# Performance work log

Hardware: AMD Instinct MI355X
Metric: run time of the kernel (lower is better)

The kernel has to match this reference:

```python
import jax, jax.numpy as jnp
import numpy as np
import math
from jax import lax

NUM_POS = 128        # random_choice in pos_neg_sampling
NUM_TOT = 256        # pos + (128 + negative_padding) always totals 256
POS_W = 10.0         # positive_weight in compute_loss


def _conv(x, w, b, pad):
    y = lax.conv_general_dilated(x, w, (1, 1), pad,
                                 dimension_numbers=('NCHW', 'OIHW', 'NCHW'))
    return y + b[None, :, None, None]


def make_anchor_box(img_h, img_w, gh, gw):
    # torch.range(0, W, W/(gw-1)) == inclusive linspace with gw points
    xs = jnp.linspace(0.0, float(img_w), gw)
    ys = jnp.linspace(0.0, float(img_h), gh)
    gx, gy = jnp.meshgrid(xs, ys, indexing='ij')          # (gw, gh) like torch.meshgrid
    xy = jnp.stack([gx.reshape(-1), gy.reshape(-1)], -1).reshape(gh, gw, 2)
    whs = []
    for area in (128 * 128, 256 * 256, 512 * 512):
        for wr, hr in ((1, 1), (2, 1), (1, 2)):
            u = math.sqrt(area / (wr * hr))
            whs.append((wr * u, hr * u))
    wh = jnp.asarray(whs, jnp.float32)                    # (9, 2)
    xy9 = jnp.broadcast_to(xy[:, :, None, :], (gh, gw, 9, 2))
    wh9 = jnp.broadcast_to(wh[None, None], (gh, gw, 9, 2))
    boxes = jnp.concatenate([xy9, xy9 + wh9], -1)         # x1,y1,x2,y2
    return boxes.reshape(-1, 4)


def pairwise_iou(t, a):
    # t: [T,4], a: [A,4], xyxy -> [T,A]
    lt = jnp.maximum(t[:, None, :2], a[None, :, :2])
    rb = jnp.minimum(t[:, None, 2:], a[None, :, 2:])
    wh = jnp.clip(rb - lt, 0.0)
    inter = wh[..., 0] * wh[..., 1]
    at = (t[:, 2] - t[:, 0]) * (t[:, 3] - t[:, 1])
    aa = (a[:, 2] - a[:, 0]) * (a[:, 3] - a[:, 1])
    return inter / (at[:, None] + aa[None, :] - inter)


def box_encode(anchor, bbox):
    awh = anchor[:, 2:] - anchor[:, :2]
    bwh = bbox[:, 2:] - bbox[:, :2]
    ac = anchor[:, :2] + awh / 2
    bc = bbox[:, :2] + bwh / 2
    dxy = (bc - ac) / awh
    dwh = jnp.log(bwh / awh)
    return jnp.concatenate([dxy, dwh], 1)


def rpn_forward(x, target, conv_w, conv_b, bbox_w, bbox_b, score_w, score_b,
                img_h, img_w):
    gh, gw = x.shape[-2], x.shape[-1]
    h = jax.nn.relu(_conv(x[None], conv_w, conv_b, 'SAME'))
    bbox = jax.nn.relu(_conv(h, bbox_w, bbox_b, 'VALID')).reshape(-1, 4)   # [A,4]
    score = jax.nn.relu(_conv(h, score_w, score_b, 'VALID')).reshape(-1, 2)  # [A,2]
    anchors = make_anchor_box(img_h, img_w, gh, gw)                        # [A,4]

    iou = pairwise_iou(target, anchors)                                    # [T,A]
    max_iou = iou.max(0)
    tgt_idx = jnp.argmax(iou, 0)

    # deterministic replacement for np.random.choice sampling (fixed shapes)
    pos_score = jnp.where(max_iou > 0.7, max_iou, -1.0)
    pos_vals, pos_idx = lax.top_k(pos_score, NUM_POS)
    pos_valid = pos_vals > 0.0
    n_pos = jnp.sum(pos_valid.astype(jnp.int32))

    neg_score = jnp.where(max_iou < 0.3, 1.0 - max_iou, -1.0)
    neg_vals, neg_idx = lax.top_k(neg_score, NUM_TOT)
    neg_valid = (neg_vals > 0.0) & (jnp.arange(NUM_TOT) < (NUM_TOT - n_pos))

    bbox_pred = bbox[pos_idx]                                              # [128,4]
    scores_sel = score[jnp.concatenate([pos_idx, neg_idx])]                # [384,2]
    valid = jnp.concatenate([pos_valid, neg_valid]).astype(jnp.float32)

    tgt_scores = jnp.concatenate([
        jnp.tile(jnp.asarray([[1.0, 0.0]], jnp.float32), (NUM_POS, 1)),
        jnp.tile(jnp.asarray([[0.0, 1.0]], jnp.float32), (NUM_TOT, 1))], 0)

    matched = target[tgt_idx[pos_idx]]
    treg = box_encode(anchors[pos_idx], matched)

    ce = -jnp.sum(tgt_scores * jax.nn.log_softmax(scores_sel, -1), -1)
    score_loss = jnp.sum(ce * valid) / jnp.maximum(jnp.sum(valid), 1.0)

    d = bbox_pred - treg
    sl1 = jnp.where(jnp.abs(d) < 1.0, 0.5 * d * d, jnp.abs(d) - 0.5)
    pm = pos_valid.astype(jnp.float32)[:, None]
    reg_loss = jnp.sum(sl1 * pm) / jnp.maximum(jnp.sum(pm) * 4.0, 1.0)

    return score_loss + POS_W * reg_loss


def setup_inputs():
    key = jax.random.key(0)
    ks = jax.random.split(key, 8)
    cin, gh, gw, nt = 512, 128, 128, 64
    x = jax.random.normal(ks[0], (cin, gh, gw), jnp.float32)
    cxy = jax.random.uniform(ks[1], (nt, 2), minval=300.0, maxval=1748.0)
    wh = jax.random.uniform(ks[2], (nt, 2), minval=64.0, maxval=512.0)
    target = jnp.concatenate([cxy - wh / 2, cxy + wh / 2], -1)
    conv_w = jax.random.normal(ks[3], (cin, cin, 3, 3), jnp.float32) * 0.02
    conv_b = jnp.zeros((cin,), jnp.float32)
    bbox_w = jax.random.normal(ks[4], (36, cin, 1, 1), jnp.float32) * 0.02
    bbox_b = jnp.zeros((36,), jnp.float32)
    score_w = jax.random.normal(ks[5], (18, cin, 1, 1), jnp.float32) * 0.02
    score_b = jnp.zeros((18,), jnp.float32)
    return {'x': x, 'target': target, 'conv_w': conv_w, 'conv_b': conv_b,
            'bbox_w': bbox_w, 'bbox_b': bbox_b, 'score_w': score_w,
            'score_b': score_b, 'img_h': 2048, 'img_w': 2048}


def reference(x, target, conv_w, conv_b, bbox_w, bbox_b, score_w, score_b,
              img_h, img_w):
    return rpn_forward(x, target, conv_w, conv_b, bbox_w, bbox_b,
                       score_w, score_b, img_h, img_w)
```

## Files before the change

kernel.cpp:

```cpp
#include <hip/hip_runtime.h>
#include <cstdint>
#include <cstddef>

typedef unsigned long long ull;
typedef __bf16 bf16x8 __attribute__((ext_vector_type(8)));
typedef float f32x4 __attribute__((ext_vector_type(4)));

#define NA     147456
#define NT     64
#define KDIM   4608
#define NTASK  1280
#define CAND_CAP 4096
#define KSPLIT 2
#define NSTEP  72
#define NIOUB  576
#define NTRB   2048
#define NPREP2 512
#define NZERO  197

#define OFF_WB2   0
#define OFF_XT    4718592
#define OFF_ZERO  22024192
#define OFF_H4    22302720
#define OFF_MIOU  32788480
#define OFF_CAND  33378304
#define OFF_CPB   34557952
#define OFF_CBZ   34560256
#define OFF_NPOS  34562560
#define OFF_TREG  34562576
#define OFF_TASKS 34564624

#define UANC 90.509667991878f
__device__ __constant__ float WKa[9] = {128.0f, 2.0f*UANC, UANC, 256.0f, 4.0f*UANC, 2.0f*UANC, 512.0f, 8.0f*UANC, 4.0f*UANC};
__device__ __constant__ float HKa[9] = {128.0f, UANC, 2.0f*UANC, 256.0f, 2.0f*UANC, 4.0f*UANC, 512.0f, 4.0f*UANC, 8.0f*UANC};

__device__ __forceinline__ float iou_one(float x1, float y1, float x2, float y2, float4 t) {
#pragma clang fp contract(off)
  float ltx = fmaxf(t.x, x1), lty = fmaxf(t.y, y1);
  float rbx = fminf(t.z, x2), rby = fminf(t.w, y2);
  float wx = fmaxf(rbx - ltx, 0.0f);
  float wy = fmaxf(rby - lty, 0.0f);
  float inter = wx * wy;
  float at = (t.z - t.x) * (t.w - t.y);
  float aa = (x2 - x1) * (y2 - y1);
  return inter / ((at + aa) - inter);
}

__device__ __forceinline__ unsigned short f2bf(float f) {
  unsigned int u = __float_as_uint(f);
  unsigned int r = (u + 0x7fffu + ((u >> 16) & 1u)) >> 16;
  return (unsigned short)r;
}

__device__ __forceinline__ int boff(int kcb) {
  int rk = kcb >> 6;
  int dy = (rk * 11) >> 5;
  int dxo = rk - dy * 3;
  return (dy * 130 + dxo) * 512 + (kcb & 63) * 8;
}

__global__ __launch_bounds__(256) void k_pi(const float* __restrict__ cw,
    unsigned short* __restrict__ Wb2, const float* __restrict__ x,
    unsigned short* __restrict__ xtb, unsigned short* __restrict__ zrg,
    const float* __restrict__ tgt, const int* __restrict__ imw,
    const int* __restrict__ imh, float* __restrict__ miou,
    ull* __restrict__ cand, int* __restrict__ cpb, int* __restrict__ cbz,
    float* __restrict__ out0) {
  __shared__ __align__(16) char smem[20480];
  int blk = blockIdx.x;
  int tid = threadIdx.x;
  if (blk >= NIOUB + NTRB + NPREP2) {
    int g = (blk - (NIOUB + NTRB + NPREP2)) * 256 + tid;
    uint4 z = {0u, 0u, 0u, 0u};
    if (g == 0) *out0 = 0.0f;
    if (g < 17408) {
      *(uint4*)(zrg + g * 8) = z;
    } else {
      int h = g - 17408;
      int pixi = h >> 6, j = h & 63;
      int yy, xx;
      if (pixi < 260) { yy = (pixi < 130) ? 0 : 129; xx = (pixi < 130) ? pixi : pixi - 130; }
      else { int p2 = pixi - 260; if (p2 < 128) { yy = 1 + p2; xx = 0; } else { yy = p2 - 127; xx = 129; } }
      *(uint4*)(xtb + (size_t)(yy * 130 + xx) * 512 + j * 8) = z;
    }
    return;
  }
  if (blk >= NIOUB + NTRB) {
    float* row = (float*)smem;
    int m = blk - (NIOUB + NTRB);
    const float* src = cw + (size_t)m * KDIM;
    for (int f = tid; f < KDIM; f += 256) {
      int cin = f / 9;
      row[cin * 10 + (f - cin * 9)] = src[f];
    }
    __syncthreads();
    for (int kc = tid; kc < 576; kc += 256) {
      int r = kc >> 6, c8 = kc & 63;
      int base = c8 * 80 + r;
      unsigned short o[8];
      #pragma unroll
      for (int j = 0; j < 8; ++j) o[j] = f2bf(row[base + j * 10]);
      *(uint4*)(Wb2 + ((size_t)kc * 512 + m) * 8) = *(const uint4*)o;
    }
    return;
  }
  if (blk >= NIOUB) {
    float* tile = (float*)smem;
    int tb = blk - NIOUB;
    int pix0 = (tb & 255) * 64;
    int cin0 = (tb >> 8) * 64;
    int pr = tid & 15, cr = tid >> 4;
    #pragma unroll
    for (int i = 0; i < 4; ++i) {
      int cin = cr + i * 16;
      float4 v = *(const float4*)(x + (size_t)(cin0 + cin) * 16384 + pix0 + pr * 4);
      tile[cin * 65 + pr * 4 + 0] = v.x;
      tile[cin * 65 + pr * 4 + 1] = v.y;
      tile[cin * 65 + pr * 4 + 2] = v.z;
      tile[cin * 65 + pr * 4 + 3] = v.w;
    }
    __syncthreads();
    #pragma unroll
    for (int i = 0; i < 4; ++i) {
      int pix = cr + i * 16;
      int plin = pix0 + pix;
      int py = plin >> 7, px = plin & 127;
      unsigned short o[4] = {f2bf(tile[(pr * 4 + 0) * 65 + pix]),
                             f2bf(tile[(pr * 4 + 1) * 65 + pix]),
                             f2bf(tile[(pr * 4 + 2) * 65 + pix]),
                             f2bf(tile[(pr * 4 + 3) * 65 + pix])};
      *(uint2*)(xtb + (size_t)((py + 1) * 130 + (px + 1)) * 512 + cin0 + pr * 4) = *(const uint2*)o;
    }
    return;
  }
  float4* ts = (float4*)smem;
  int* wz = (int*)(smem + 1024);
  int* wc = wz + 4;
  if (tid < NT) ts[tid] = ((const float4*)tgt)[tid];
  __syncthreads();
  int a = blk * 256 + tid;
  int k = a % 9;
  int pq = a / 9;
  int p = pq >> 7, q = pq & 127;
  float dx = (float)(*imw) / 127.0f;
  float dyl = (float)(*imh) / 127.0f;
  float x1 = (float)p * dx, y1 = (float)q * dyl;
  float x2 = x1 + WKa[k], y2 = y1 + HKa[k];
  float best = -1.0f;
  #pragma unroll 8
  for (int t = 0; t < NT; ++t) best = fmaxf(best, iou_one(x1, y1, x2, y2, ts[t]));
  miou[a] = best;
  int lane = tid & 63, w = tid >> 6;
  ull bz = __ballot(best == 0.0f);
  bool isc = best > 0.7f;
  ull bc = __ballot(isc);
  if (lane == 0) { wz[w] = (int)__popcll(bz); wc[w] = (int)__popcll(bc); }
  __syncthreads();
  if (tid == 0) {
    cbz[blk] = wz[0] + wz[1] + wz[2] + wz[3];
    cpb[blk] = wc[0] + wc[1] + wc[2] + wc[3];
  }
  if (isc) {
    int woff = 0;
    for (int i = 0; i < w; ++i) woff += wc[i];
    int rank = woff + (int)__popcll(bc & ((1ull << lane) - 1ull));
    cand[blk * 256 + rank] = ((ull)__float_as_uint(best) << 32) | (ull)(0xFFFFFFFFu - (unsigned)a);
  }
}

__global__ __launch_bounds__(256) void k_mfma(const unsigned short* __restrict__ Wb2,
    const unsigned short* __restrict__ xtb, unsigned short* __restrict__ zrg,
    const ull* __restrict__ cand, const int* __restrict__ cpb,
    const float* __restrict__ miou, const int* __restrict__ cbz,
    const float* __restrict__ tgt, const int* __restrict__ imw,
    const int* __restrict__ imh,
    int* __restrict__ nposp, float* __restrict__ treg, int* __restrict__ tasks,
    float* __restrict__ H4) {
  __shared__ ull keys[CAND_CAP];
  __shared__ ull bnd[1024];
  __shared__ int hist[1024];
  __shared__ int cpbL[576];
  __shared__ int base576[577];
  __shared__ int wtot[4];
  __shared__ int selCnt, bndCnt, Tbin, mAbove;
  __shared__ int posi[128];
  __shared__ int npS;
  __shared__ int nzbase[145];
  __shared__ float4 ts[NT];
  __shared__ int negA[256];
  __shared__ int wsum[4];

  int tid = threadIdx.x;
  int* flag = (int*)zrg;
  bool isSel = (blockIdx.x == 9 && blockIdx.y == 3 && blockIdx.z == 1);

  if (isSel) {
    int lane = tid & 63;
    if (tid < NT) ts[tid] = ((const float4*)tgt)[tid];
    for (int i = tid; i < 576; i += 256) cpbL[i] = cpb[i];
    for (int i = tid; i < 1024; i += 256) hist[i] = 0;
    __syncthreads();
    int e0 = 0, e1 = 0, sA = 0, scanA = 0;
    if (tid < 192) {
      e0 = cpbL[3 * tid]; e1 = cpbL[3 * tid + 1]; int e2 = cpbL[3 * tid + 2];
      sA = e0 + e1 + e2;
      scanA = sA;
      for (int off = 1; off < 64; off <<= 1) {
        int v = __shfl_up(scanA, off);
        if (lane >= off) scanA += v;
      }
      if (lane == 63) wtot[tid >> 6] = scanA;
    }
    __syncthreads();
    if (tid < 192) {
      int w = tid >> 6;
      int woff = 0;
      for (int i = 0; i < w; ++i) woff += wtot[i];
      int excl = woff + scanA - sA;
      base576[3 * tid]     = excl;
      base576[3 * tid + 1] = excl + e0;
      base576[3 * tid + 2] = excl + e0 + e1;
      if (tid == 191) base576[576] = excl + sA;
    }
    __syncthreads();
    int cnt = base576[576]; if (cnt > CAND_CAP) cnt = CAND_CAP;
    for (int i = tid; i < CAND_CAP; i += 256) if (i >= cnt) keys[i] = 0ull;
    for (int rk = tid; rk < cnt; rk += 256) {
      int lo = 0, hi = 576;
      while (hi - lo > 1) { int mid = (lo + hi) >> 1; if (base576[mid] <= rk) lo = mid; else hi = mid; }
      keys[rk] = cand[lo * 256 + (rk - base576[lo])];
    }
    __syncthreads();
    if (cnt <= 128) {
      if (tid < cnt) posi[tid] = (int)(0xFFFFFFFFu - (unsigned)(keys[tid] & 0xFFFFFFFFull));
      if (tid == 0) { npS = cnt; *nposp = cnt; }
    } else {
      for (int i = tid; i < cnt; i += 256) {
        unsigned ib = (unsigned)(keys[i] >> 32);
        atomicAdd(&hist[(ib - 0x3F333334u) >> 13], 1);
      }
      __syncthreads();
      if (tid < 64) {
        int s = 0;
        #pragma unroll
        for (int t = 0; t < 16; ++t) s += hist[tid * 16 + t];
        int S = s;
        #pragma unroll
        for (int off = 1; off < 64; off <<= 1) {
          int u = __shfl_down(S, off);
          if (tid + off < 64) S += u;
        }
        ull mask = __ballot(S >= 128);
        int g = 63 - __clzll(mask);
        int aboveS = __shfl(S, (g + 1 < 64) ? g + 1 : 63);
        if (g == 63) aboveS = 0;
        if (tid == 0) {
          int run = aboveS, T = g * 16 + 15;
          for (int b = g * 16 + 15; b >= g * 16; --b) {
            int h = hist[b];
            if (run + h >= 128) { T = b; break; }
            run += h;
          }
          Tbin = T; mAbove = run; selCnt = 0; bndCnt = 0;
        }
      }
      __syncthreads();
      int T = Tbin, m = mAbove;
      for (int i = tid; i < cnt; i += 256) {
        ull kk = keys[i];
        unsigned ib = (unsigned)(kk >> 32);
        int b = (int)((ib - 0x3F333334u) >> 13);
        if (b > T) {
          int r = atomicAdd(&selCnt, 1);
          posi[r] = (int)(0xFFFFFFFFu - (unsigned)(kk & 0xFFFFFFFFull));
        } else if (b == T) {
          int r = atomicAdd(&bndCnt, 1);
          if (r < 1024) bnd[r] = kk;
        }
      }
      __syncthreads();
      int B = bndCnt;
      int need = 128 - m;
      if (B <= 1024) {
        int n2 = 2; while (n2 < B) n2 <<= 1;
        for (int i = tid; i < n2; i += 256) if (i >= B) bnd[i] = 0ull;
        for (int size = 2; size <= n2; size <<= 1)
          for (int stride = size >> 1; stride > 0; stride >>= 1) {
            __syncthreads();
            for (int t = tid; t < n2 / 2; t += 256) {
              int i = 2 * t - (t & (stride - 1));
              int j = i + stride;
              ull a = bnd[i], b2 = bnd[j];
              bool desc = ((i & size) == 0);
              if (desc ? (a < b2) : (a > b2)) { bnd[i] = b2; bnd[j] = a; }
            }
          }
        __syncthreads();
        if (tid < need) posi[m + tid] = (int)(0xFFFFFFFFu - (unsigned)(bnd[tid] & 0xFFFFFFFFull));
      } else {
        for (int size = 2; size <= CAND_CAP; size <<= 1)
          for (int stride = size >> 1; stride > 0; stride >>= 1) {
            __syncthreads();
            for (int t = tid; t < CAND_CAP / 2; t += 256) {
              int i = 2 * t - (t & (stride - 1));
              int j = i + stride;
              ull a = keys[i], b2 = keys[j];
              bool desc = ((i & size) == 0);
              if (desc ? (a < b2) : (a > b2)) { keys[i] = b2; keys[j] = a; }
            }
          }
        __syncthreads();
        if (tid < 128) posi[tid] = (int)(0xFFFFFFFFu - (unsigned)(keys[tid] & 0xFFFFFFFFull));
      }
      if (tid == 0) { npS = 128; *nposp = 128; }
    }
    __syncthreads();
    int np = npS;
    int sB = 0, scanB = 0;
    if (tid < 144) {
      int4 cz4 = *(const int4*)(cbz + 4 * tid);
      sB = cz4.x + cz4.y + cz4.z + cz4.w;
      scanB = sB;
      for (int off = 1; off < 64; off <<= 1) {
        int v = __shfl_up(scanB, off);
        if (lane >= off) scanB += v;
      }
      bool last = (tid < 128) ? (lane == 63) : (tid == 143);
      if (last) wsum[tid >> 6] = scanB;
    }
    __syncthreads();
    if (tid < 144) {
      int w = tid >> 6;
      int woff = 0;
      for (int i = 0; i < w; ++i) woff += wsum[i];
      nzbase[tid] = woff + scanB - sB;
      if (tid == 143) nzbase[144] = woff + scanB;
    }
    __syncthreads();
    int w = tid >> 6;
    for (int j = 0; j < 144; ++j) {
      if (nzbase[j] >= 256) break;
      int a0 = j * 1024 + tid * 4;
      float4 m4 = *(const float4*)(miou + a0);
      int f0 = (m4.x == 0.0f), f1 = (m4.y == 0.0f), f2 = (m4.z == 0.0f), f3 = (m4.w == 0.0f);
      int tsum = f0 + f1 + f2 + f3;
      int scan = tsum;
      for (int off = 1; off < 64; off <<= 1) {
        int v = __shfl_up(scan, off);
        if (lane >= off) scan += v;
      }
      if (lane == 63) wsum[w] = scan;
      __syncthreads();
      int woff = nzbase[j];
      for (int i = 0; i < w; ++i) woff += wsum[i];
      int r = woff + scan - tsum;
      if (f0) { if (r < 256) negA[r] = a0;     r++; }
      if (f1) { if (r < 256) negA[r] = a0 + 1; r++; }
      if (f2) { if (r < 256) negA[r] = a0 + 2; r++; }
      if (f3) { if (r < 256) negA[r] = a0 + 3;      }
      __syncthreads();
    }
    __syncthreads();
    if (tid < np) {
      int a = posi[tid];
      int k = a % 9; int pq = a / 9; int p = pq >> 7, q = pq & 127;
      float dx = (float)(*imw) / 127.0f, dyl = (float)(*imh) / 127.0f;
      float x1 = (float)p * dx, y1 = (float)q * dyl;
      float x2 = x1 + WKa[k], y2 = y1 + HKa[k];
      float best = -1.0f; int bt = 0;
      for (int t = 0; t < NT; ++t) {
        float v = iou_one(x1, y1, x2, y2, ts[t]);
        if (v > best) { best = v; bt = t; }
      }
      float4 m = ts[bt];
      float aw = x2 - x1, ah = y2 - y1;
      float acx = x1 + aw * 0.5f, acy = y1 + ah * 0.5f;
      float bwd = m.z - m.x, bhd = m.w - m.y;
      float bcx = m.x + bwd * 0.5f, bcy = m.y + bhd * 0.5f;
      treg[tid * 4 + 0] = (bcx - acx) / aw;
      treg[tid * 4 + 1] = (bcy - acy) / ah;
      treg[tid * 4 + 2] = logf(bwd / aw);
      treg[tid * 4 + 3] = logf(bhd / ah);
    }
    for (int t = tid; t < NTASK; t += 256) {
      int rec = 0;
      if (t < 768) {
        int s = t / 6, jj = t - s * 6;
        if (s < np) {
          int a = posi[s];
          int f, wr, xx;
          if (jj < 4) { f = 4 * a; wr = f >> 14; xx = (f & 127) + jj; }
          else        { f = 2 * a; wr = 36 + (f >> 14); xx = (f & 127) + (jj - 4); }
          int yy = (f >> 7) & 127;
          rec = (int)(0x80000000u | ((unsigned)wr << 16) | ((unsigned)yy << 8) | (unsigned)xx);
        }
      } else {
        int s = (t - 768) >> 1, jj = (t - 768) & 1;
        if (s < 256 - np) {
          int a = negA[s];
          int f = 2 * a; int wr = 36 + (f >> 14); int yy = (f >> 7) & 127; int xx = (f & 127) + jj;
          rec = (int)(0x80000000u | ((unsigned)wr << 16) | ((unsigned)yy << 8) | (unsigned)xx);
        }
      }
      tasks[t] = rec;
    }
    __threadfence();
    __syncthreads();
    if (tid == 0) atomicExch(flag, 1);
  } else {
    int c0p = blockIdx.y * 128;
    int kbase = blockIdx.z * 288;
    unsigned accp = 0;
    for (int i = tid; i < 288 * 32; i += 256) {
      int kc = i >> 5, mq = (i & 31) * 4;
      accp ^= *(const unsigned*)(Wb2 + ((size_t)(kbase + kc) * 512 + c0p + mq) * 8);
    }
    asm volatile("" :: "v"(accp));
    if (tid == 0) {
      while (atomicCAS(flag, 2, 2) == 0) __builtin_amdgcn_s_sleep(32);
    }
    __syncthreads();
    __threadfence();
  }

  int npos = *nposp;
  int tt0 = blockIdx.x * 128;
  int posend = 6 * npos, negend = 768 + 2 * (256 - npos);
  if (!((tt0 < posend) || ((tt0 + 128 > 768) && (tt0 < negend)))) return;
  int c0 = blockIdx.y * 128;
  int ks = blockIdx.z;
  int wave = tid >> 6, lane = tid & 63;
  int quad = lane >> 4, r = lane & 15;
  int m_base = c0 + (wave & 1) * 64;
  int n_base = tt0 + (wave >> 1) * 64;
  int kc0 = ks * 288 + quad;
  const bf16x8* Ab = (const bf16x8*)Wb2 + ((size_t)kc0 * 512 + m_base + r);

  const unsigned short* Bp[4];
  #pragma unroll
  for (int ni = 0; ni < 4; ++ni) {
    int rec = tasks[n_base + ni * 16 + r];
    int pix = (rec < 0) ? (((rec >> 8) & 127) * 130 + (rec & 127)) : 0;
    const unsigned short* base = (rec < 0) ? xtb : zrg;
    Bp[ni] = base + (size_t)pix * 512 + quad * 8;
  }
  int kcb = ks * 288;

  f32x4 acc[4][4];
  #pragma unroll
  for (int i = 0; i < 4; ++i)
    #pragma unroll
    for (int j = 0; j < 4; ++j) acc[i][j] = (f32x4){0.f, 0.f, 0.f, 0.f};

  bf16x8 a[4], b[4];
  #pragma unroll
  for (int mi = 0; mi < 4; ++mi) a[mi] = Ab[mi * 16];
  int ob0 = boff(kcb);
  #pragma unroll
  for (int ni = 0; ni < 4; ++ni) b[ni] = *(const bf16x8*)(Bp[ni] + ob0);

  for (int s = 0; s < NSTEP; ++s) {
    bf16x8 an[4], bn[4];
    if (s < NSTEP - 1) {
      const bf16x8* An = Ab + (size_t)(s + 1) * 4 * 512;
      int ob = boff(kcb + 4 * (s + 1));
      #pragma unroll
      for (int mi = 0; mi < 4; ++mi) an[mi] = An[mi * 16];
      #pragma unroll
      for (int ni = 0; ni < 4; ++ni) bn[ni] = *(const bf16x8*)(Bp[ni] + ob);
    }
    #pragma unroll
    for (int mi = 0; mi < 4; ++mi)
      #pragma unroll
      for (int ni = 0; ni < 4; ++ni)
        acc[mi][ni] = __builtin_amdgcn_mfma_f32_16x16x32_bf16(a[mi], b[ni], acc[mi][ni], 0, 0, 0);
    if (s < NSTEP - 1) {
      #pragma unroll
      for (int mi = 0; mi < 4; ++mi) a[mi] = an[mi];
      #pragma unroll
      for (int ni = 0; ni < 4; ++ni) b[ni] = bn[ni];
    }
  }
  size_t hb = (size_t)ks * NTASK;
  #pragma unroll
  for (int mi = 0; mi < 4; ++mi) {
    int c = m_base + mi * 16 + quad * 4;
    #pragma unroll
    for (int ni = 0; ni < 4; ++ni) {
      int t = n_base + ni * 16 + r;
      *(f32x4*)(H4 + (hb + t) * 512 + c) = acc[mi][ni];
    }
  }
}

__global__ __launch_bounds__(256) void k_out(const float* __restrict__ H4,
    const int* __restrict__ tasks,
    const float* __restrict__ cb, const float* __restrict__ bw,
    const float* __restrict__ bb, const float* __restrict__ sw,
    const float* __restrict__ sb, const float* __restrict__ treg,
    const int* __restrict__ nposp, float* __restrict__ out) {
  __shared__ float sOut[4];
  __shared__ float sContrib[4];
  int wave = threadIdx.x >> 6, lane = threadIdx.x & 63;
  int t = blockIdx.x * 4 + wave;
  int rec = tasks[t];
  float outval = 0.0f;
  if (rec < 0) {
    int wr = (rec >> 16) & 63;
    const float* wrow = (wr < 36) ? (bw + wr * 512) : (sw + (wr - 36) * 512);
    float s = 0.0f;
    #pragma unroll
    for (int it = 0; it < 8; ++it) {
      int c = it * 64 + lane;
      size_t o = (size_t)t * 512 + c;
      float hv = H4[o] + H4[o + 1280 * 512] + cb[c];
      s = fmaf(fmaxf(hv, 0.0f), wrow[c], s);
    }
    #pragma unroll
    for (int off = 32; off > 0; off >>= 1) s += __shfl_down(s, off);
    if (lane == 0) {
      float b = (wr < 36) ? bb[wr] : sb[wr - 36];
      outval = fmaxf(s + b, 0.0f);
    }
  }
  if (lane == 0) sOut[wave] = outval;
  __syncthreads();
  if (lane == 0) {
    float contrib = 0.0f;
    if (rec < 0) {
      if (t < 768) {
        int s6 = t / 6, j = t - s6 * 6;
        if (j < 4) {
          int np = *nposp;
          float d = outval - treg[s6 * 4 + j];
          float ad = fabsf(d);
          float sl1 = (ad < 1.0f) ? 0.5f * d * d : ad - 0.5f;
          contrib = 10.0f * sl1 / fmaxf(4.0f * (float)np, 1.0f);
        } else if (j == 4) {
          float s0 = outval, s1 = sOut[wave + 1];
          float mm = fmaxf(s0, s1);
          float lse = mm + logf(expf(s0 - mm) + expf(s1 - mm));
          contrib = (lse - s0) * (1.0f / 256.0f);
        }
      } else if (((t - 768) & 1) == 0) {
        float s0 = outval, s1 = sOut[wave + 1];
        float mm = fmaxf(s0, s1);
        float lse = mm + logf(expf(s0 - mm) + expf(s1 - mm));
        contrib = (lse - s1) * (1.0f / 256.0f);
      }
    }
    sContrib[wave] = contrib;
  }
  __syncthreads();
  if (threadIdx.x == 0) {
    float c = sContrib[0] + sContrib[1] + sContrib[2] + sContrib[3];
    if (c != 0.0f) atomicAdd(out, c);
  }
}

extern "C" void kernel_launch(void* const* d_in, const int* in_sizes, int n_in,
                              void* d_out, int out_size, void* d_ws, size_t ws_size,
                              hipStream_t stream) {
  const float* x   = (const float*)d_in[0];
  const float* tgt = (const float*)d_in[1];
  const float* cw  = (const float*)d_in[2];
  const float* cb  = (const float*)d_in[3];
  const float* bw  = (const float*)d_in[4];
  const float* bb  = (const float*)d_in[5];
  const float* sw  = (const float*)d_in[6];
  const float* sb  = (const float*)d_in[7];
  const int* imh   = (const int*)d_in[8];
  const int* imw   = (const int*)d_in[9];

  char* ws = (char*)d_ws;
  unsigned short* Wb2 = (unsigned short*)(ws + OFF_WB2);
  unsigned short* xtb = (unsigned short*)(ws + OFF_XT);
  unsigned short* zrg = (unsigned short*)(ws + OFF_ZERO);
  float* H4    = (float*)(ws + OFF_H4);
  float* miou  = (float*)(ws + OFF_MIOU);
  ull*   cand  = (ull*)(ws + OFF_CAND);
  int*   cpb   = (int*)(ws + OFF_CPB);
  int*   cbz   = (int*)(ws + OFF_CBZ);
  int*   nposp = (int*)(ws + OFF_NPOS);
  float* treg  = (float*)(ws + OFF_TREG);
  int*   tasks = (int*)(ws + OFF_TASKS);
  float* out   = (float*)d_out;

  k_pi   <<<dim3(NIOUB + NTRB + NPREP2 + NZERO), dim3(256), 0, stream>>>(cw, Wb2, x, xtb, zrg, tgt, imw, imh, miou, cand, cpb, cbz, out);
  k_mfma <<<dim3(10, 4, KSPLIT),  dim3(256), 0, stream>>>(Wb2, xtb, zrg, cand, cpb, miou, cbz, tgt, imw, imh, nposp, treg, tasks, H4);
  k_out  <<<dim3(320),            dim3(256), 0, stream>>>(H4, tasks, cb, bw, bb, sw, sb, treg, nposp, out);
}
```

Before: 179.9 us.

## Split selection block into separate single-block kernel launch

Moves the positive/negative sample selection, which ran inside one designated block of the MFMA kernel, into its own single-block kernel launched before the MFMA kernel. The other blocks no longer prefetch weights into cache and spin on a global flag waiting for the selector. This removes the flag handshake and its dependence on co-scheduling. In exchange it adds a kernel launch boundary and loses the overlap between selection and the weight warm-up.

```diff
diff --git a/kernel.cpp b/kernel.cpp
--- a/kernel.cpp
+++ b/kernel.cpp
@@ -168,14 +168,11 @@
   }
 }
 
-__global__ __launch_bounds__(256) void k_mfma(const unsigned short* __restrict__ Wb2,
-    const unsigned short* __restrict__ xtb, unsigned short* __restrict__ zrg,
-    const ull* __restrict__ cand, const int* __restrict__ cpb,
-    const float* __restrict__ miou, const int* __restrict__ cbz,
-    const float* __restrict__ tgt, const int* __restrict__ imw,
-    const int* __restrict__ imh,
-    int* __restrict__ nposp, float* __restrict__ treg, int* __restrict__ tasks,
-    float* __restrict__ H4) {
+__global__ __launch_bounds__(256) void k_sel(const ull* __restrict__ cand,
+    const int* __restrict__ cpb, const float* __restrict__ miou,
+    const int* __restrict__ cbz, const float* __restrict__ tgt,
+    const int* __restrict__ imw, const int* __restrict__ imh,
+    int* __restrict__ nposp, float* __restrict__ treg, int* __restrict__ tasks) {
   __shared__ ull keys[CAND_CAP];
   __shared__ ull bnd[1024];
   __shared__ int hist[1024];
@@ -189,246 +186,229 @@
   __shared__ float4 ts[NT];
   __shared__ int negA[256];
   __shared__ int wsum[4];
-
   int tid = threadIdx.x;
-  int* flag = (int*)zrg;
-  bool isSel = (blockIdx.x == 9 && blockIdx.y == 3 && blockIdx.z == 1);
-
-  if (isSel) {
-    int lane = tid & 63;
-    if (tid < NT) ts[tid] = ((const float4*)tgt)[tid];
-    for (int i = tid; i < 576; i += 256) cpbL[i] = cpb[i];
-    for (int i = tid; i < 1024; i += 256) hist[i] = 0;
-    __syncthreads();
-    int e0 = 0, e1 = 0, sA = 0, scanA = 0;
-    if (tid < 192) {
-      e0 = cpbL[3 * tid]; e1 = cpbL[3 * tid + 1]; int e2 = cpbL[3 * tid + 2];
-      sA = e0 + e1 + e2;
-      scanA = sA;
+  int lane = tid & 63;
+  if (tid < NT) ts[tid] = ((const float4*)tgt)[tid];
+  for (int i = tid; i < 576; i += 256) cpbL[i] = cpb[i];
+  for (int i = tid; i < 1024; i += 256) hist[i] = 0;
+  __syncthreads();
+  int e0 = 0, e1 = 0, sA = 0, scanA = 0;
+  if (tid < 192) {
+    e0 = cpbL[3 * tid]; e1 = cpbL[3 * tid + 1]; int e2 = cpbL[3 * tid + 2];
+    sA = e0 + e1 + e2;
+    scanA = sA;
+    for (int off = 1; off < 64; off <<= 1) {
+      int v = __shfl_up(scanA, off);
+      if (lane >= off) scanA += v;
+    }
+    if (lane == 63) wtot[tid >> 6] = scanA;
+  }
+  __syncthreads();
+  if (tid < 192) {
+    int w = tid >> 6;
+    int woff = 0;
+    for (int i = 0; i < w; ++i) woff += wtot[i];
+    int excl = woff + scanA - sA;
+    base576[3 * tid]     = excl;
+    base576[3 * tid + 1] = excl + e0;
+    base576[3 * tid + 2] = excl + e0 + e1;
+    if (tid == 191) base576[576] = excl + sA;
+  }
+  __syncthreads();
+  int cnt = base576[576]; if (cnt > CAND_CAP) cnt = CAND_CAP;
+  for (int i = tid; i < CAND_CAP; i += 256) if (i >= cnt) keys[i] = 0ull;
+  for (int rk = tid; rk < cnt; rk += 256) {
+    int lo = 0, hi = 576;
+    while (hi - lo > 1) { int mid = (lo + hi) >> 1; if (base576[mid] <= rk) lo = mid; else hi = mid; }
+    keys[rk] = cand[lo * 256 + (rk - base576[lo])];
+  }
+  __syncthreads();
+  if (cnt <= 128) {
+    if (tid < cnt) posi[tid] = (int)(0xFFFFFFFFu - (unsigned)(keys[tid] & 0xFFFFFFFFull));
+    if (tid == 0) { npS = cnt; *nposp = cnt; }
+  } else {
+    for (int i = tid; i < cnt; i += 256) {
+      unsigned ib = (unsigned)(keys[i] >> 32);
+      atomicAdd(&hist[(ib - 0x3F333334u) >> 13], 1);
+    }
+    __syncthreads();
+    if (tid < 64) {
+      int s = 0;
+      #pragma unroll
+      for (int t = 0; t < 16; ++t) s += hist[tid * 16 + t];
+      int S = s;
+      #pragma unroll
       for (int off = 1; off < 64; off <<= 1) {
-        int v = __shfl_up(scanA, off);
-        if (lane >= off) scanA += v;
+        int u = __shfl_down(S, off);
+        if (tid + off < 64) S += u;
       }
-      if (lane == 63) wtot[tid >> 6] = scanA;
-    }
-    __syncthreads();
-    if (tid < 192) {
-      int w = tid >> 6;
-      int woff = 0;
-      for (int i = 0; i < w; ++i) woff += wtot[i];
-      int excl = woff + scanA - sA;
-      base576[3 * tid]     = excl;
-      base576[3 * tid + 1] = excl + e0;
-      base576[3 * tid + 2] = excl + e0 + e1;
-      if (tid == 191) base576[576] = excl + sA;
-    }
-    __syncthreads();
-    int cnt = base576[576]; if (cnt > CAND_CAP) cnt = CAND_CAP;
-    for (int i = tid; i < CAND_CAP; i += 256) if (i >= cnt) keys[i] = 0ull;
-    for (int rk = tid; rk < cnt; rk += 256) {
-      int lo = 0, hi = 576;
-      while (hi - lo > 1) { int mid = (lo + hi) >> 1; if (base576[mid] <= rk) lo = mid; else hi = mid; }
-      keys[rk] = cand[lo * 256 + (rk - base576[lo])];
-    }
-    __syncthreads();
-    if (cnt <= 128) {
-      if (tid < cnt) posi[tid] = (int)(0xFFFFFFFFu - (unsigned)(keys[tid] & 0xFFFFFFFFull));
-      if (tid == 0) { npS = cnt; *nposp = cnt; }
+      ull mask = __ballot(S >= 128);
+      int g = 63 - __clzll(mask);
+      int aboveS = __shfl(S, (g + 1 < 64) ? g + 1 : 63);
+      if (g == 63) aboveS = 0;
+      if (tid == 0) {
+        int run = aboveS, T = g * 16 + 15;
+        for (int b = g * 16 + 15; b >= g * 16; --b) {
+          int h = hist[b];
+          if (run + h >= 128) { T = b; break; }
+          run += h;
+        }
+        Tbin = T; mAbove = run; selCnt = 0; bndCnt = 0;
+      }
+    }
+    __syncthreads();
+    int T = Tbin, m = mAbove;
+    for (int i = tid; i < cnt; i += 256) {
+      ull kk = keys[i];
+      unsigned ib = (unsigned)(kk >> 32);
+      int b = (int)((ib - 0x3F333334u) >> 13);
+      if (b > T) {
+        int r = atomicAdd(&selCnt, 1);
+        posi[r] = (int)(0xFFFFFFFFu - (unsigned)(kk & 0xFFFFFFFFull));
+      } else if (b == T) {
+        int r = atomicAdd(&bndCnt, 1);
+        if (r < 1024) bnd[r] = kk;
+      }
+    }
+    __syncthreads();
+    int B = bndCnt;
+    int need = 128 - m;
+    if (B <= 1024) {
+      int n2 = 2; while (n2 < B) n2 <<= 1;
+      for (int i = tid; i < n2; i += 256) if (i >= B) bnd[i] = 0ull;
+      for (int size = 2; size <= n2; size <<= 1)
+        for (int stride = size >> 1; stride > 0; stride >>= 1) {
+          __syncthreads();
+          for (int t = tid; t < n2 / 2; t += 256) {
+            int i = 2 * t - (t & (stride - 1));
+            int j = i + stride;
+            ull a = bnd[i], b2 = bnd[j];
+            bool desc = ((i & size) == 0);
+            if (desc ? (a < b2) : (a > b2)) { bnd[i] = b2; bnd[j] = a; }
+          }
+        }
+      __syncthreads();
+      if (tid < need) posi[m + tid] = (int)(0xFFFFFFFFu - (unsigned)(bnd[tid] & 0xFFFFFFFFull));
     } else {
-      for (int i = tid; i < cnt; i += 256) {
-        unsigned ib = (unsigned)(keys[i] >> 32);
-        atomicAdd(&hist[(ib - 0x3F333334u) >> 13], 1);
+      for (int size = 2; size <= CAND_CAP; size <<= 1)
+        for (int stride = size >> 1; stride > 0; stride >>= 1) {
+          __syncthreads();
+          for (int t = tid; t < CAND_CAP / 2; t += 256) {
+            int i = 2 * t - (t & (stride - 1));
+            int j = i + stride;
+            ull a = keys[i], b2 = keys[j];
+            bool desc = ((i & size) == 0);
+            if (desc ? (a < b2) : (a > b2)) { keys[i] = b2; keys[j] = a; }
+          }
+        }
+      __syncthreads();
+      if (tid < 128) posi[tid] = (int)(0xFFFFFFFFu - (unsigned)(keys[tid] & 0xFFFFFFFFull));
+    }
+    if (tid == 0) { npS = 128; *nposp = 128; }
+  }
+  __syncthreads();
+  int np = npS;
+  int sB = 0, scanB = 0;
+  if (tid < 144) {
+    int4 cz4 = *(const int4*)(cbz + 4 * tid);
+    sB = cz4.x + cz4.y + cz4.z + cz4.w;
+    scanB = sB;
+    for (int off = 1; off < 64; off <<= 1) {
+      int v = __shfl_up(scanB, off);
+      if (lane >= off) scanB += v;
+    }
+    bool last = (tid < 128) ? (lane == 63) : (tid == 143);
+    if (last) wsum[tid >> 6] = scanB;
+  }
+  __syncthreads();
+  if (tid < 144) {
+    int w = tid >> 6;
+    int woff = 0;
+    for (int i = 0; i < w; ++i) woff += wsum[i];
+    nzbase[tid] = woff + scanB - sB;
+    if (tid == 143) nzbase[144] = woff + scanB;
+  }
+  __syncthreads();
+  int w = tid >> 6;
+  for (int j = 0; j < 144; ++j) {
+    if (nzbase[j] >= 256) break;
+    int a0 = j * 1024 + tid * 4;
+    float4 m4 = *(const float4*)(miou + a0);
+    int f0 = (m4.x == 0.0f), f1 = (m4.y == 0.0f), f2 = (m4.z == 0.0f), f3 = (m4.w == 0.0f);
+    int tsum = f0 + f1 + f2 + f3;
+    int scan = tsum;
+    for (int off = 1; off < 64; off <<= 1) {
+      int v = __shfl_up(scan, off);
+      if (lane >= off) scan += v;
+    }
+    if (lane == 63) wsum[w] = scan;
+    __syncthreads();
+    int woff = nzbase[j];
+    for (int i = 0; i < w; ++i) woff += wsum[i];
+    int r = woff + scan - tsum;
+    if (f0) { if (r < 256) negA[r] = a0;     r++; }
+    if (f1) { if (r < 256) negA[r] = a0 + 1; r++; }
+    if (f2) { if (r < 256) negA[r] = a0 + 2; r++; }
+    if (f3) { if (r < 256) negA[r] = a0 + 3;      }
+    __syncthreads();
+  }
+  __syncthreads();
+  if (tid < np) {
+    int a = posi[tid];
+    int k = a % 9; int pq = a / 9; int p = pq >> 7, q = pq & 127;
+    float dx = (float)(*imw) / 127.0f, dyl = (float)(*imh) / 127.0f;
+    float x1 = (float)p * dx, y1 = (float)q * dyl;
+    float x2 = x1 + WKa[k], y2 = y1 + HKa[k];
+    float best = -1.0f; int bt = 0;
+    for (int t = 0; t < NT; ++t) {
+      float v = iou_one(x1, y1, x2, y2, ts[t]);
+      if (v > best) { best = v; bt = t; }
+    }
+    float4 m = ts[bt];
+    float aw = x2 - x1, ah = y2 - y1;
+    float acx = x1 + aw * 0.5f, acy = y1 + ah * 0.5f;
+    float bwd = m.z - m.x, bhd = m.w - m.y;
+    float bcx = m.x + bwd * 0.5f, bcy = m.y + bhd * 0.5f;
+    treg[tid * 4 + 0] = (bcx - acx) / aw;
+    treg[tid * 4 + 1] = (bcy - acy) / ah;
+    treg[tid * 4 + 2] = logf(bwd / aw);
+    treg[tid * 4 + 3] = logf(bhd / ah);
+  }
+  for (int t = tid; t < NTASK; t += 256) {
+    int rec = 0;
+    if (t < 768) {
+      int s = t / 6, jj = t - s * 6;
+      if (s < np) {
+        int a = posi[s];
+        int f, wr, xx;
+        if (jj < 4) { f = 4 * a; wr = f >> 14; xx = (f & 127) + jj; }
+        else        { f = 2 * a; wr = 36 + (f >> 14); xx = (f & 127) + (jj - 4); }
+        int yy = (f >> 7) & 127;
+        rec = (int)(0x80000000u | ((unsigned)wr << 16) | ((unsigned)yy << 8) | (unsigned)xx);
       }
-      __syncthreads();
-      if (tid < 64) {
-        int s = 0;
-        #pragma unroll
-        for (int t = 0; t < 16; ++t) s += hist[tid * 16 + t];
-        int S = s;
-        #pragma unroll
-        for (int off = 1; off < 64; off <<= 1) {
-          int u = __shfl_down(S, off);
-          if (tid + off < 64) S += u;
-        }
-        ull mask = __ballot(S >= 128);
-        int g = 63 - __clzll(mask);
-        int aboveS = __shfl(S, (g + 1 < 64) ? g + 1 : 63);
-        if (g == 63) aboveS = 0;
-        if (tid == 0) {
-          int run = aboveS, T = g * 16 + 15;
-          for (int b = g * 16 + 15; b >= g * 16; --b) {
-            int h = hist[b];
-            if (run + h >= 128) { T = b; break; }
-            run += h;
-          }
-          Tbin = T; mAbove = run; selCnt = 0; bndCnt = 0;
-        }
+    } else {
+      int s = (t - 768) >> 1, jj = (t - 768) & 1;
+      if (s < 256 - np) {
+        int a = negA[s];
+        int f = 2 * a; int wr = 36 + (f >> 14); int yy = (f >> 7) & 127; int xx = (f & 127) + jj;
+        rec = (int)(0x80000000u | ((unsigned)wr << 16) | ((unsigned)yy << 8) | (unsigned)xx);
       }
-      __syncthreads();
-      int T = Tbin, m = mAbove;
-      for (int i = tid; i < cnt; i += 256) {
-        ull kk = keys[i];
-        unsigned ib = (unsigned)(kk >> 32);
-        int b = (int)((ib - 0x3F333334u) >> 13);
-        if (b > T) {
-          int r = atomicAdd(&selCnt, 1);
-          posi[r] = (int)(0xFFFFFFFFu - (unsigned)(kk & 0xFFFFFFFFull));
-        } else if (b == T) {
-          int r = atomicAdd(&bndCnt, 1);
-          if (r < 1024) bnd[r] = kk;
-        }
-      }
-      __syncthreads();
-      int B = bndCnt;
-      int need = 128 - m;
-      if (B <= 1024) {
-        int n2 = 2; while (n2 < B) n2 <<= 1;
-        for (int i = tid; i < n2; i += 256) if (i >= B) bnd[i] = 0ull;
-        for (int size = 2; size <= n2; size <<= 1)
-          for (int stride = size >> 1; stride > 0; stride >>= 1) {
-            __syncthreads();
-            for (int t = tid; t < n2 / 2; t += 256) {
-              int i = 2 * t - (t & (stride - 1));
-              int j = i + stride;
-              ull a = bnd[i], b2 = bnd[j];
-              bool desc = ((i & size) == 0);
-              if (desc ? (a < b2) : (a > b2)) { bnd[i] = b2; bnd[j] = a; }
-            }
-          }
-        __syncthreads();
-        if (tid < need) posi[m + tid] = (int)(0xFFFFFFFFu - (unsigned)(bnd[tid] & 0xFFFFFFFFull));
-      } else {
-        for (int size = 2; size <= CAND_CAP; size <<= 1)
-          for (int stride = size >> 1; stride > 0; stride >>= 1) {
-            __syncthreads();
-            for (int t = tid; t < CAND_CAP / 2; t += 256) {
-              int i = 2 * t - (t & (stride - 1));
-              int j = i + stride;
-              ull a = keys[i], b2 = keys[j];
-              bool desc = ((i & size) == 0);
-              if (desc ? (a < b2) : (a > b2)) { keys[i] = b2; keys[j] = a; }
-            }
-          }
-        __syncthreads();
-        if (tid < 128) posi[tid] = (int)(0xFFFFFFFFu - (unsigned)(keys[tid] & 0xFFFFFFFFull));
-      }
-      if (tid == 0) { npS = 128; *nposp = 128; }
-    }
-    __syncthreads();
-    int np = npS;
-    int sB = 0, scanB = 0;
-    if (tid < 144) {
-      int4 cz4 = *(const int4*)(cbz + 4 * tid);
-      sB = cz4.x + cz4.y + cz4.z + cz4.w;
-      scanB = sB;
-      for (int off = 1; off < 64; off <<= 1) {
-        int v = __shfl_up(scanB, off);
-        if (lane >= off) scanB += v;
-      }
-      bool last = (tid < 128) ? (lane == 63) : (tid == 143);
-      if (last) wsum[tid >> 6] = scanB;
-    }
-    __syncthreads();
-    if (tid < 144) {
-      int w = tid >> 6;
-      int woff = 0;
-      for (int i = 0; i < w; ++i) woff += wsum[i];
-      nzbase[tid] = woff + scanB - sB;
-      if (tid == 143) nzbase[144] = woff + scanB;
-    }
-    __syncthreads();
-    int w = tid >> 6;
-    for (int j = 0; j < 144; ++j) {
-      if (nzbase[j] >= 256) break;
-      int a0 = j * 1024 + tid * 4;
-      float4 m4 = *(const float4*)(miou + a0);
-      int f0 = (m4.x == 0.0f), f1 = (m4.y == 0.0f), f2 = (m4.z == 0.0f), f3 = (m4.w == 0.0f);
-      int tsum = f0 + f1 + f2 + f3;
-      int scan = tsum;
-      for (int off = 1; off < 64; off <<= 1) {
-        int v = __shfl_up(scan, off);
-        if (lane >= off) scan += v;
-      }
-      if (lane == 63) wsum[w] = scan;
-      __syncthreads();
-      int woff = nzbase[j];
-      for (int i = 0; i < w; ++i) woff += wsum[i];
-      int r = woff + scan - tsum;
-      if (f0) { if (r < 256) negA[r] = a0;     r++; }
-      if (f1) { if (r < 256) negA[r] = a0 + 1; r++; }
-      if (f2) { if (r < 256) negA[r] = a0 + 2; r++; }
-      if (f3) { if (r < 256) negA[r] = a0 + 3;      }
-      __syncthreads();
-    }
-    __syncthreads();
-    if (tid < np) {
-      int a = posi[tid];
-      int k = a % 9; int pq = a / 9; int p = pq >> 7, q = pq & 127;
-      float dx = (float)(*imw) / 127.0f, dyl = (float)(*imh) / 127.0f;
-      float x1 = (float)p * dx, y1 = (float)q * dyl;
-      float x2 = x1 + WKa[k], y2 = y1 + HKa[k];
-      float best = -1.0f; int bt = 0;
-      for (int t = 0; t < NT; ++t) {
-        float v = iou_one(x1, y1, x2, y2, ts[t]);
-        if (v > best) { best = v; bt = t; }
-      }
-      float4 m = ts[bt];
-      float aw = x2 - x1, ah = y2 - y1;
-      float acx = x1 + aw * 0.5f, acy = y1 + ah * 0.5f;
-      float bwd = m.z - m.x, bhd = m.w - m.y;
-      float bcx = m.x + bwd * 0.5f, bcy = m.y + bhd * 0.5f;
-      treg[tid * 4 + 0] = (bcx - acx) / aw;
-      treg[tid * 4 + 1] = (bcy - acy) / ah;
-      treg[tid * 4 + 2] = logf(bwd / aw);
-      treg[tid * 4 + 3] = logf(bhd / ah);
-    }
-    for (int t = tid; t < NTASK; t += 256) {
-      int rec = 0;
-      if (t < 768) {
-        int s = t / 6, jj = t - s * 6;
-        if (s < np) {
-          int a = posi[s];
-          int f, wr, xx;
-          if (jj < 4) { f = 4 * a; wr = f >> 14; xx = (f & 127) + jj; }
-          else        { f = 2 * a; wr = 36 + (f >> 14); xx = (f & 127) + (jj - 4); }
-          int yy = (f >> 7) & 127;
-          rec = (int)(0x80000000u | ((unsigned)wr << 16) | ((unsigned)yy << 8) | (unsigned)xx);
-        }
-      } else {
-        int s = (t - 768) >> 1, jj = (t - 768) & 1;
-        if (s < 256 - np) {
-          int a = negA[s];
-          int f = 2 * a; int wr = 36 + (f >> 14); int yy = (f >> 7) & 127; int xx = (f & 127) + jj;
-          rec = (int)(0x80000000u | ((unsigned)wr << 16) | ((unsigned)yy << 8) | (unsigned)xx);
-        }
-      }
-      tasks[t] = rec;
-    }
-    __threadfence();
-    __syncthreads();
-    if (tid == 0) atomicExch(flag, 1);
-  } else {
-    int c0p = blockIdx.y * 128;
-    int kbase = blockIdx.z * 288;
-    unsigned accp = 0;
-    for (int i = tid; i < 288 * 32; i += 256) {
-      int kc = i >> 5, mq = (i & 31) * 4;
-      accp ^= *(const unsigned*)(Wb2 + ((size_t)(kbase + kc) * 512 + c0p + mq) * 8);
-    }
-    asm volatile("" :: "v"(accp));
-    if (tid == 0) {
-      while (atomicCAS(flag, 2, 2) == 0) __builtin_amdgcn_s_sleep(32);
-    }
-    __syncthreads();
-    __threadfence();
-  }
-
+    }
+    tasks[t] = rec;
+  }
+}
+
+__global__ __launch_bounds__(256) void k_mfma(const unsigned short* __restrict__ Wb2,
+    const unsigned short* __restrict__ xtb, const unsigned short* __restrict__ zrg,
+    const int* __restrict__ tasks, const int* __restrict__ nposp,
+    float* __restrict__ H4) {
   int npos = *nposp;
   int tt0 = blockIdx.x * 128;
   int posend = 6 * npos, negend = 768 + 2 * (256 - npos);
   if (!((tt0 < posend) || ((tt0 + 128 > 768) && (tt0 < negend)))) return;
   int c0 = blockIdx.y * 128;
   int ks = blockIdx.z;
+  int tid = threadIdx.x;
   int wave = tid >> 6, lane = tid & 63;
   int quad = lane >> 4, r = lane & 15;
   int m_base = c0 + (wave & 1) * 64;
@@ -587,6 +567,7 @@
   float* out   = (float*)d_out;
 
   k_pi   <<<dim3(NIOUB + NTRB + NPREP2 + NZERO), dim3(256), 0, stream>>>(cw, Wb2, x, xtb, zrg, tgt, imw, imh, miou, cand, cpb, cbz, out);
-  k_mfma <<<dim3(10, 4, KSPLIT),  dim3(256), 0, stream>>>(Wb2, xtb, zrg, cand, cpb, miou, cbz, tgt, imw, imh, nposp, treg, tasks, H4);
+  k_sel  <<<dim3(1),              dim3(256), 0, stream>>>(cand, cpb, miou, cbz, tgt, imw, imh, nposp, treg, tasks);
+  k_mfma <<<dim3(10, 4, KSPLIT),  dim3(256), 0, stream>>>(Wb2, xtb, zrg, tasks, nposp, H4);
   k_out  <<<dim3(320),            dim3(256), 0, stream>>>(H4, tasks, cb, bw, bb, sw, sb, treg, nposp, out);
 }
```

Measured after the change: 175.6 us. 2.4% less time.
